# Performance work log

Measured on AMD Instinct MI355X. Metric: run time of the kernel, lower is better.

## Reference

```python
import jax, jax.numpy as jnp
import numpy as np

DIM = 2048
HEADS = 16
DIM_HEAD = 128
FF_MULT = 4
ATTN_INNER = HEADS * DIM_HEAD            # 2048
FF_INNER = DIM * FF_MULT                 # 8192
FUSED = ATTN_INNER + DIM_HEAD + DIM_HEAD + 2 * FF_INNER  # 18688
B, N = 2, 2048


def setup_inputs() -> dict:
    key = jax.random.key(0)
    k0, k1, k2, k3 = jax.random.split(key, 4)
    s = lambda fan_in: 1.0 / np.sqrt(fan_in)
    return {
        "x": jax.random.normal(k0, (B, N, DIM), jnp.float32),
        "gamma": jnp.ones((DIM,), jnp.float32),
        "beta": jnp.zeros((DIM,), jnp.float32),
        "w_fused": jax.random.normal(k1, (DIM, FUSED), jnp.float32) * s(DIM),
        "w_attn_out": jax.random.normal(k2, (ATTN_INNER, DIM), jnp.float32) * s(ATTN_INNER),
        "w_ff_out": jax.random.normal(k3, (FF_INNER, DIM), jnp.float32) * s(FF_INNER),
    }


def _rotate_half(t):
    t1, t2 = jnp.split(t, 2, axis=-1)
    return jnp.concatenate([-t2, t1], axis=-1)


def _rope(pos, t):
    # pos: [n, d] broadcast over leading dims of t (..., n, d)
    return t * jnp.cos(pos) + _rotate_half(t) * jnp.sin(pos)


def reference(x, gamma, beta, w_fused, w_attn_out, w_ff_out):
    b, n, d = x.shape
    # LayerNorm (eps = 1e-5, matching F.layer_norm default)
    mu = jnp.mean(x, axis=-1, keepdims=True)
    var = jnp.var(x, axis=-1, keepdims=True)
    h = (x - mu) * jax.lax.rsqrt(var + 1e-5) * gamma + beta

    # Fused projection feeding attention (multi-query) and parallel SwiGLU FF
    proj = h @ w_fused  # [b, n, FUSED]
    i0 = ATTN_INNER
    i1 = i0 + DIM_HEAD
    i2 = i1 + DIM_HEAD
    q, k, v, ff = jnp.split(proj, [i0, i1, i2], axis=-1)
    q = q.reshape(b, n, HEADS, DIM_HEAD).transpose(0, 2, 1, 3)  # [b, h, n, dh]

    # Rotary embedding: freqs duplicated, rotate-half application
    inv_freq = 1.0 / (10000.0 ** (jnp.arange(0, DIM_HEAD, 2, dtype=jnp.float32) / DIM_HEAD))
    freqs = jnp.arange(n, dtype=jnp.float32)[:, None] * inv_freq[None, :]
    pos = jnp.concatenate([freqs, freqs], axis=-1)  # [n, dh]
    q = _rope(pos, q)          # [b, h, n, dh]
    k = _rope(pos, k)          # [b, n, dh] (single KV head)

    # Multi-query causal attention
    scale = 1.0 / jnp.sqrt(jnp.asarray(DIM_HEAD, q.dtype))
    sim = jnp.einsum('bhid,bjd->bhij', q, k) * scale  # [b, h, n, n]
    causal = jnp.triu(jnp.ones((n, n), dtype=bool), 1)
    sim = jnp.where(causal, jnp.finfo(sim.dtype).min, sim)
    attn = jax.nn.softmax(sim, axis=-1)
    out = jnp.einsum('bhij,bjd->bhid', attn, v)       # [b, h, n, dh]
    out = out.transpose(0, 2, 1, 3).reshape(b, n, ATTN_INNER)

    # Parallel SwiGLU FF: chunk -> silu(gate) * x
    x_ff, gate = jnp.split(ff, 2, axis=-1)  # each [b, n, FF_INNER]
    ff_o = (jax.nn.silu(gate) * x_ff) @ w_ff_out

    return out @ w_attn_out + ff_o
```

## Files before the change

### kernel.cpp

```cpp
#include <hip/hip_runtime.h>
#include <hip/hip_bf16.h>
#include <math.h>

#define DIM 2048
#define HEADS 16
#define DH 128
#define ATTN_INNER 2048
#define FF_INNER 8192
#define FUSED_N 18688
#define QKV_N 2304
#define BATCH 2
#define SEQ 2048
#define ROWS (BATCH*SEQ)

typedef __attribute__((ext_vector_type(8))) __bf16 bf16x8;
typedef __attribute__((ext_vector_type(4))) float f32x4;

typedef __attribute__((address_space(1))) void* as1_void;
typedef __attribute__((address_space(3))) void* as3_void;

__device__ __forceinline__ void async16(const void* g, void* l) {
  __builtin_amdgcn_global_load_lds((as1_void)const_cast<void*>(g), (as3_void)l, 16, 0, 0);
}

__global__ __launch_bounds__(256) void ln_kernel(const float* __restrict__ x,
                                                 const float* __restrict__ gamma,
                                                 const float* __restrict__ beta,
                                                 __hip_bfloat16* __restrict__ hb) {
  const int row = blockIdx.x;
  const int t = threadIdx.x;
  const float4* x4 = (const float4*)(x + (size_t)row * DIM);
  float4 a = x4[t];
  float4 c = x4[t + 256];
  float s  = a.x + a.y + a.z + a.w + c.x + c.y + c.z + c.w;
  float ss = a.x*a.x + a.y*a.y + a.z*a.z + a.w*a.w +
             c.x*c.x + c.y*c.y + c.z*c.z + c.w*c.w;
  for (int off = 32; off > 0; off >>= 1) {
    s  += __shfl_down(s, off);
    ss += __shfl_down(ss, off);
  }
  __shared__ float red[8];
  int wv = t >> 6, lane = t & 63;
  if (lane == 0) { red[wv] = s; red[wv + 4] = ss; }
  __syncthreads();
  s  = red[0] + red[1] + red[2] + red[3];
  ss = red[4] + red[5] + red[6] + red[7];
  float mu  = s * (1.0f / DIM);
  float var = ss * (1.0f / DIM) - mu * mu;
  float rs  = rsqrtf(var + 1e-5f);
  __hip_bfloat16* o = hb + (size_t)row * DIM;
  float v0[4] = {a.x, a.y, a.z, a.w};
  float v1[4] = {c.x, c.y, c.z, c.w};
#pragma unroll
  for (int i = 0; i < 4; i++) {
    int c0 = t * 4 + i;
    int c1 = 1024 + t * 4 + i;
    o[c0] = __float2bfloat16((v0[i] - mu) * rs * gamma[c0] + beta[c0]);
    o[c1] = __float2bfloat16((v1[i] - mu) * rs * gamma[c1] + beta[c1]);
  }
}

__global__ __launch_bounds__(256) void tcvt_kernel(const float* __restrict__ src,
                                                   __hip_bfloat16* __restrict__ dst,
                                                   int R, int C) {
  __shared__ float tile[64][65];
  const int cb = blockIdx.x * 64, rb = blockIdx.y * 64;
  const int t = threadIdx.x;
  const int tc = t & 63, tr = t >> 6;
#pragma unroll
  for (int i = 0; i < 16; i++) {
    int r = tr + i * 4;
    tile[r][tc] = src[(size_t)(rb + r) * C + cb + tc];
  }
  __syncthreads();
#pragma unroll
  for (int i = 0; i < 16; i++) {
    int c = tr + i * 4;
    dst[(size_t)(cb + c) * R + rb + tc] = __float2bfloat16(tile[tc][c]);
  }
}

__global__ __launch_bounds__(256) void tbf16_kernel(const __hip_bfloat16* __restrict__ src, int lds_,
                                                    __hip_bfloat16* __restrict__ dst, int ldd,
                                                    int R, int C) {
  __shared__ __hip_bfloat16 tile[64][65];
  const int cb = blockIdx.x * 64, rb = blockIdx.y * 64;
  const int t = threadIdx.x;
  const int tc = t & 63, tr = t >> 6;
#pragma unroll
  for (int i = 0; i < 16; i++) {
    int r = tr + i * 4;
    tile[r][tc] = src[(size_t)(rb + r) * lds_ + cb + tc];
  }
  __syncthreads();
#pragma unroll
  for (int i = 0; i < 16; i++) {
    int c = tr + i * 4;
    dst[(size_t)(cb + c) * ldd + rb + tc] = tile[tc][c];
  }
}

__global__ __launch_bounds__(256) void rope_kernel(__hip_bfloat16* __restrict__ qkv) {
  const size_t tid = (size_t)blockIdx.x * 256 + threadIdx.x;
  const int d = tid & 63;
  const int u = (tid >> 6) % 17;
  const int row = tid / (17 * 64);
  const int n = row & (SEQ - 1);
  size_t base = (size_t)row * QKV_N + (u < 16 ? u * DH : ATTN_INNER);
  float inv = powf(10000.0f, -(float)d * (1.0f / 64.0f));
  float th = (float)n * inv;
  float cs = cosf(th), sn = sinf(th);
  float a = __bfloat162float(qkv[base + d]);
  float b = __bfloat162float(qkv[base + d + 64]);
  qkv[base + d]      = __float2bfloat16(a * cs - b * sn);
  qkv[base + d + 64] = __float2bfloat16(b * cs + a * sn);
}

template<int EPI>
__global__ __launch_bounds__(256) void gemm_bt(const __hip_bfloat16* __restrict__ A, int lda,
                                               const __hip_bfloat16* __restrict__ Bt, int ldb,
                                               void* __restrict__ Cptr, int ldc, int K) {
  __shared__ __hip_bfloat16 As[128 * 32];
  __shared__ __hip_bfloat16 Bs[128 * 32];
  const int tid = threadIdx.x;
  const int wv = tid >> 6, lane = tid & 63;
  const int quad = lane >> 4, l15 = lane & 15;
  const int m0 = blockIdx.y * 128, n0 = blockIdx.x * 128;
  const int wm = (wv >> 1) * 64, wn = (wv & 1) * 64;

  f32x4 acc[4][4];
#pragma unroll
  for (int i = 0; i < 4; i++)
#pragma unroll
    for (int j = 0; j < 4; j++) acc[i][j] = (f32x4){0.f, 0.f, 0.f, 0.f};

  for (int k0 = 0; k0 < K; k0 += 32) {
#pragma unroll
    for (int j = 0; j < 2; j++) {
      int q = wv * 2 + j;
      int e = q * 512 + lane * 8;
      int row = e >> 5, col = e & 31;
      async16(A  + (size_t)(m0 + row) * lda + k0 + col, As + q * 512);
      async16(Bt + (size_t)(n0 + row) * ldb + k0 + col, Bs + q * 512);
    }
    __syncthreads();
    bf16x8 af[4], bfr[4];
#pragma unroll
    for (int i = 0; i < 4; i++)
      af[i] = *(const bf16x8*)(As + (wm + i * 16 + l15) * 32 + quad * 8);
#pragma unroll
    for (int j = 0; j < 4; j++)
      bfr[j] = *(const bf16x8*)(Bs + (wn + j * 16 + l15) * 32 + quad * 8);
#pragma unroll
    for (int i = 0; i < 4; i++)
#pragma unroll
      for (int j = 0; j < 4; j++)
        acc[i][j] = __builtin_amdgcn_mfma_f32_16x16x32_bf16(af[i], bfr[j], acc[i][j], 0, 0, 0);
    __syncthreads();
  }

  if constexpr (EPI == 0 || EPI == 1) {
    __hip_bfloat16* C = (__hip_bfloat16*)Cptr;
#pragma unroll
    for (int i = 0; i < 4; i++) {
      int rowb = m0 + wm + i * 16 + quad * 4;
#pragma unroll
      for (int j = 0; j < 4; j++) {
        int col = n0 + wn + j * 16 + l15;
#pragma unroll
        for (int r = 0; r < 4; r++) {
          float v = acc[i][j][r];
          size_t idx = (size_t)(rowb + r) * ldc + col;
          if constexpr (EPI == 1) {
            float xf = __bfloat162float(C[idx]);
            v = v / (1.0f + expf(-v)) * xf;
          }
          C[idx] = __float2bfloat16(v);
        }
      }
    }
  } else {
    float* C = (float*)Cptr;
#pragma unroll
    for (int i = 0; i < 4; i++) {
      int rowb = m0 + wm + i * 16 + quad * 4;
#pragma unroll
      for (int j = 0; j < 4; j++) {
        int col = n0 + wn + j * 16 + l15;
#pragma unroll
        for (int r = 0; r < 4; r++) {
          size_t idx = (size_t)(rowb + r) * ldc + col;
          if constexpr (EPI == 3) C[idx] += acc[i][j][r];
          else                    C[idx]  = acc[i][j][r];
        }
      }
    }
  }
}

__global__ __launch_bounds__(256) void flash_kernel(const __hip_bfloat16* __restrict__ qkv,
                                                    const __hip_bfloat16* __restrict__ vt,
                                                    __hip_bfloat16* __restrict__ aob) {
  __shared__ __hip_bfloat16 Qs[128 * 128];
  __shared__ __hip_bfloat16 Ks[64 * 128];
  __shared__ __hip_bfloat16 Vts[128 * 64];
  __shared__ __hip_bfloat16 Ps[128 * 64];

  const int blk = blockIdx.x;
  const int bh = blk & 31;
  const int qi = blk >> 5;
  const int qt = (qi & 1) ? (qi >> 1) : (15 - (qi >> 1));
  const int bat = bh >> 4, h = bh & 15;

  const int tid = threadIdx.x;
  const int wv = tid >> 6, lane = tid & 63;
  const int quad = lane >> 4, l15 = lane & 15;
  const float scale = 0.08838834764831845f;

#pragma unroll
  for (int j = 0; j < 8; j++) {
    int is = wv * 8 + j;
    int e = is * 512 + lane * 8;
    int r = e >> 7, c = e & 127;
    async16(qkv + (size_t)(bat * SEQ + qt * 128 + r) * QKV_N + h * DH + c, Qs + is * 512);
  }

  f32x4 oacc[2][8];
#pragma unroll
  for (int i = 0; i < 2; i++)
#pragma unroll
    for (int j = 0; j < 8; j++) oacc[i][j] = (f32x4){0.f, 0.f, 0.f, 0.f};
  float mrow[2][4], lrow[2][4];
#pragma unroll
  for (int i = 0; i < 2; i++)
#pragma unroll
    for (int r = 0; r < 4; r++) { mrow[i][r] = -INFINITY; lrow[i][r] = 0.f; }

  const int jt_max = 2 * qt + 1;
  for (int jt = 0; jt <= jt_max; jt++) {
    __syncthreads();
#pragma unroll
    for (int j = 0; j < 4; j++) {
      int is = wv * 4 + j;
      int e = is * 512 + lane * 8;
      { int r = e >> 7, c = e & 127;
        async16(qkv + (size_t)(bat * SEQ + jt * 64 + r) * QKV_N + ATTN_INNER + c, Ks + is * 512); }
      { int d = e >> 6, jc = e & 63;
        async16(vt + (size_t)d * ROWS + bat * SEQ + jt * 64 + jc, Vts + is * 512); }
    }
    __syncthreads();

    f32x4 sacc[2][4];
#pragma unroll
    for (int i = 0; i < 2; i++)
#pragma unroll
      for (int j = 0; j < 4; j++) sacc[i][j] = (f32x4){0.f, 0.f, 0.f, 0.f};
#pragma unroll
    for (int kq = 0; kq < 4; kq++) {
      bf16x8 qa[2], kb[4];
#pragma unroll
      for (int i = 0; i < 2; i++)
        qa[i] = *(const bf16x8*)(Qs + (wv * 32 + i * 16 + l15) * 128 + kq * 32 + quad * 8);
#pragma unroll
      for (int j = 0; j < 4; j++)
        kb[j] = *(const bf16x8*)(Ks + (j * 16 + l15) * 128 + kq * 32 + quad * 8);
#pragma unroll
      for (int i = 0; i < 2; i++)
#pragma unroll
        for (int j = 0; j < 4; j++)
          sacc[i][j] = __builtin_amdgcn_mfma_f32_16x16x32_bf16(qa[i], kb[j], sacc[i][j], 0, 0, 0);
    }

#pragma unroll
    for (int i = 0; i < 2; i++) {
#pragma unroll
      for (int r = 0; r < 4; r++) {
        int row_g = qt * 128 + wv * 32 + i * 16 + quad * 4 + r;
        float mt = -INFINITY;
#pragma unroll
        for (int j = 0; j < 4; j++) {
          int col_g = jt * 64 + j * 16 + l15;
          float sv = sacc[i][j][r] * scale;
          if (col_g > row_g) sv = -INFINITY;
          sacc[i][j][r] = sv;
          mt = fmaxf(mt, sv);
        }
#pragma unroll
        for (int off = 1; off < 16; off <<= 1) mt = fmaxf(mt, __shfl_xor(mt, off));
        float mn = fmaxf(mrow[i][r], mt);
        float al = expf(mrow[i][r] - mn);
        float rs = 0.f;
#pragma unroll
        for (int j = 0; j < 4; j++) {
          float p = expf(sacc[i][j][r] - mn);
          sacc[i][j][r] = p;
          rs += p;
        }
#pragma unroll
        for (int off = 1; off < 16; off <<= 1) rs += __shfl_xor(rs, off);
        lrow[i][r] = lrow[i][r] * al + rs;
        mrow[i][r] = mn;
#pragma unroll
        for (int i2 = 0; i2 < 8; i2++) oacc[i][i2][r] *= al;
      }
    }

#pragma unroll
    for (int i = 0; i < 2; i++)
#pragma unroll
      for (int j = 0; j < 4; j++)
#pragma unroll
        for (int r = 0; r < 4; r++)
          Ps[(wv * 32 + i * 16 + quad * 4 + r) * 64 + j * 16 + l15] =
              __float2bfloat16(sacc[i][j][r]);
    __syncthreads();

#pragma unroll
    for (int kp = 0; kp < 2; kp++) {
      bf16x8 pa[2], vb[8];
#pragma unroll
      for (int i = 0; i < 2; i++)
        pa[i] = *(const bf16x8*)(Ps + (wv * 32 + i * 16 + l15) * 64 + kp * 32 + quad * 8);
#pragma unroll
      for (int i2 = 0; i2 < 8; i2++)
        vb[i2] = *(const bf16x8*)(Vts + (i2 * 16 + l15) * 64 + kp * 32 + quad * 8);
#pragma unroll
      for (int i = 0; i < 2; i++)
#pragma unroll
        for (int i2 = 0; i2 < 8; i2++)
          oacc[i][i2] = __builtin_amdgcn_mfma_f32_16x16x32_bf16(pa[i], vb[i2], oacc[i][i2], 0, 0, 0);
    }
  }

#pragma unroll
  for (int i = 0; i < 2; i++)
#pragma unroll
    for (int r = 0; r < 4; r++) {
      float inv = 1.0f / lrow[i][r];
      int row_g = bat * SEQ + qt * 128 + wv * 32 + i * 16 + quad * 4 + r;
#pragma unroll
      for (int i2 = 0; i2 < 8; i2++)
        aob[(size_t)row_g * ATTN_INNER + h * DH + i2 * 16 + l15] =
            __float2bfloat16(oacc[i][i2][r] * inv);
    }
}

extern "C" void kernel_launch(void* const* d_in, const int* in_sizes, int n_in,
                              void* d_out, int out_size, void* d_ws, size_t ws_size,
                              hipStream_t stream) {
  const float* x       = (const float*)d_in[0];
  const float* gamma   = (const float*)d_in[1];
  const float* beta    = (const float*)d_in[2];
  const float* w_fused = (const float*)d_in[3];
  const float* w_attn  = (const float*)d_in[4];
  const float* w_ff    = (const float*)d_in[5];
  float* out = (float*)d_out;
  char* ws = (char*)d_ws;

  size_t off = 0;
  auto alloc = [&](size_t bytes) {
    size_t o = off;
    off += (bytes + 255) & ~(size_t)255;
    return o;
  };
  __hip_bfloat16* hb   = (__hip_bfloat16*)(ws + alloc((size_t)ROWS * DIM * 2));
  __hip_bfloat16* wfbt = (__hip_bfloat16*)(ws + alloc((size_t)FUSED_N * DIM * 2));
  __hip_bfloat16* qkvb = (__hip_bfloat16*)(ws + alloc((size_t)ROWS * QKV_N * 2));
  __hip_bfloat16* gb   = (__hip_bfloat16*)(ws + alloc((size_t)ROWS * FF_INNER * 2));
  __hip_bfloat16* wat  = (__hip_bfloat16*)(ws + alloc((size_t)DIM * ATTN_INNER * 2));
  __hip_bfloat16* wfot = (__hip_bfloat16*)(ws + alloc((size_t)DIM * FF_INNER * 2));
  __hip_bfloat16* vt   = (__hip_bfloat16*)(ws + alloc((size_t)DH * ROWS * 2));
  __hip_bfloat16* aob  = (__hip_bfloat16*)(ws + alloc((size_t)ROWS * ATTN_INNER * 2));

  ln_kernel<<<ROWS, 256, 0, stream>>>(x, gamma, beta, hb);

  tcvt_kernel<<<dim3(FUSED_N / 64, DIM / 64), 256, 0, stream>>>(w_fused, wfbt, DIM, FUSED_N);
  tcvt_kernel<<<dim3(DIM / 64, ATTN_INNER / 64), 256, 0, stream>>>(w_attn, wat, ATTN_INNER, DIM);
  tcvt_kernel<<<dim3(DIM / 64, FF_INNER / 64), 256, 0, stream>>>(w_ff, wfot, FF_INNER, DIM);

  gemm_bt<0><<<dim3(QKV_N / 128, ROWS / 128), 256, 0, stream>>>(hb, DIM, wfbt, DIM, qkvb, QKV_N, DIM);

  rope_kernel<<<(ROWS * 17 * 64) / 256, 256, 0, stream>>>(qkvb);

  tbf16_kernel<<<dim3(DH / 64, ROWS / 64), 256, 0, stream>>>(qkvb + ATTN_INNER + DH, QKV_N, vt, ROWS, ROWS, DH);

  flash_kernel<<<512, 256, 0, stream>>>(qkvb, vt, aob);

  gemm_bt<0><<<dim3(FF_INNER / 128, ROWS / 128), 256, 0, stream>>>(
      hb, DIM, wfbt + (size_t)QKV_N * DIM, DIM, gb, FF_INNER, DIM);
  gemm_bt<1><<<dim3(FF_INNER / 128, ROWS / 128), 256, 0, stream>>>(
      hb, DIM, wfbt + (size_t)(QKV_N + FF_INNER) * DIM, DIM, gb, FF_INNER, DIM);

  gemm_bt<2><<<dim3(DIM / 128, ROWS / 128), 256, 0, stream>>>(aob, ATTN_INNER, wat, ATTN_INNER, out, DIM, ATTN_INNER);
  gemm_bt<3><<<dim3(DIM / 128, ROWS / 128), 256, 0, stream>>>(gb, FF_INNER, wfot, FF_INNER, out, DIM, FF_INNER);

  (void)in_sizes; (void)n_in; (void)out_size; (void)ws_size;
}
```

Baseline: 1.324 ms.

## Fuse SwiGLU GEMMs and output GEMMs, add tile swizzle and wider K steps

Replaces the generic templated GEMM with three specialised kernels. The FF value and gate projections are computed in one kernel, which keeps both accumulators and applies SiLU-gating in registers, so the intermediate x_ff is never written to or read back from memory. The attention-out and FF-out projections are accumulated in one kernel, removing the fp32 output read-modify-write. It also adds grouped tile swizzling for L2 reuse, a 64-wide K step per barrier, an occupancy hint, and vectorised weight-transpose loads and stores. Together these raise register pressure, and the fused output GEMM has fewer, longer-running blocks.

```diff
diff --git a/kernel.cpp b/kernel.cpp
--- a/kernel.cpp
+++ b/kernel.cpp
@@ -21,6 +21,16 @@
 
 __device__ __forceinline__ void async16(const void* g, void* l) {
   __builtin_amdgcn_global_load_lds((as1_void)const_cast<void*>(g), (as3_void)l, 16, 0, 0);
+}
+
+__device__ __forceinline__ void swizzle_tile(int& tm, int& tn) {
+  const int num_n = gridDim.x;
+  const int pid = blockIdx.y * num_n + blockIdx.x;
+  const int group = 8 * num_n;
+  const int gid = pid / group;
+  const int rem = pid % group;
+  tm = gid * 8 + (rem % 8);
+  tn = rem / 8;
 }
 
 __global__ __launch_bounds__(256) void ln_kernel(const float* __restrict__ x,
@@ -66,17 +76,24 @@
   __shared__ float tile[64][65];
   const int cb = blockIdx.x * 64, rb = blockIdx.y * 64;
   const int t = threadIdx.x;
-  const int tc = t & 63, tr = t >> 6;
-#pragma unroll
-  for (int i = 0; i < 16; i++) {
-    int r = tr + i * 4;
-    tile[r][tc] = src[(size_t)(rb + r) * C + cb + tc];
+  const int lr = t >> 4, lc4 = (t & 15) * 4;
+#pragma unroll
+  for (int i = 0; i < 4; i++) {
+    float4 v = *(const float4*)&src[(size_t)(rb + lr + i * 16) * C + cb + lc4];
+    tile[lr + i * 16][lc4 + 0] = v.x;
+    tile[lr + i * 16][lc4 + 1] = v.y;
+    tile[lr + i * 16][lc4 + 2] = v.z;
+    tile[lr + i * 16][lc4 + 3] = v.w;
   }
   __syncthreads();
-#pragma unroll
-  for (int i = 0; i < 16; i++) {
-    int c = tr + i * 4;
-    dst[(size_t)(cb + c) * R + rb + tc] = __float2bfloat16(tile[tc][c]);
+  const int tcc = t & 31, trc = t >> 5;
+#pragma unroll
+  for (int i = 0; i < 8; i++) {
+    int c = trc + i * 8;
+    __hip_bfloat162 pk;
+    pk.x = __float2bfloat16(tile[2 * tcc][c]);
+    pk.y = __float2bfloat16(tile[2 * tcc + 1][c]);
+    *(__hip_bfloat162*)&dst[(size_t)(cb + c) * R + rb + 2 * tcc] = pk;
   }
 }
 
@@ -116,84 +133,185 @@
   qkv[base + d + 64] = __float2bfloat16(b * cs + a * sn);
 }
 
-template<int EPI>
-__global__ __launch_bounds__(256) void gemm_bt(const __hip_bfloat16* __restrict__ A, int lda,
-                                               const __hip_bfloat16* __restrict__ Bt, int ldb,
-                                               void* __restrict__ Cptr, int ldc, int K) {
-  __shared__ __hip_bfloat16 As[128 * 32];
-  __shared__ __hip_bfloat16 Bs[128 * 32];
+__global__ __launch_bounds__(256, 3) void gemm_qkv(const __hip_bfloat16* __restrict__ A,
+                                                   const __hip_bfloat16* __restrict__ Bt,
+                                                   __hip_bfloat16* __restrict__ C) {
+  __shared__ __hip_bfloat16 As[2][128 * 32];
+  __shared__ __hip_bfloat16 Bs[2][128 * 32];
   const int tid = threadIdx.x;
   const int wv = tid >> 6, lane = tid & 63;
   const int quad = lane >> 4, l15 = lane & 15;
-  const int m0 = blockIdx.y * 128, n0 = blockIdx.x * 128;
+  int tm, tn; swizzle_tile(tm, tn);
+  const int m0 = tm * 128, n0 = tn * 128;
   const int wm = (wv >> 1) * 64, wn = (wv & 1) * 64;
-
-  f32x4 acc[4][4];
-#pragma unroll
-  for (int i = 0; i < 4; i++)
-#pragma unroll
-    for (int j = 0; j < 4; j++) acc[i][j] = (f32x4){0.f, 0.f, 0.f, 0.f};
-
-  for (int k0 = 0; k0 < K; k0 += 32) {
+  const int srow = lane >> 2, scol = (lane & 3) * 8;
+
+  f32x4 acc[4][4] = {};
+  for (int k0 = 0; k0 < DIM; k0 += 64) {
+#pragma unroll
+    for (int h = 0; h < 2; h++)
+#pragma unroll
+      for (int j = 0; j < 2; j++) {
+        int q = wv * 2 + j;
+        int row = q * 16 + srow;
+        async16(A  + (size_t)(m0 + row) * DIM + k0 + h * 32 + scol, &As[h][q * 512]);
+        async16(Bt + (size_t)(n0 + row) * DIM + k0 + h * 32 + scol, &Bs[h][q * 512]);
+      }
+    __syncthreads();
+#pragma unroll
+    for (int h = 0; h < 2; h++) {
+      bf16x8 af[4], bfr[4];
+#pragma unroll
+      for (int i = 0; i < 4; i++)
+        af[i] = *(const bf16x8*)(&As[h][(wm + i * 16 + l15) * 32 + quad * 8]);
+#pragma unroll
+      for (int j = 0; j < 4; j++)
+        bfr[j] = *(const bf16x8*)(&Bs[h][(wn + j * 16 + l15) * 32 + quad * 8]);
+#pragma unroll
+      for (int i = 0; i < 4; i++)
+#pragma unroll
+        for (int j = 0; j < 4; j++)
+          acc[i][j] = __builtin_amdgcn_mfma_f32_16x16x32_bf16(af[i], bfr[j], acc[i][j], 0, 0, 0);
+    }
+    __syncthreads();
+  }
+#pragma unroll
+  for (int i = 0; i < 4; i++) {
+    int rowb = m0 + wm + i * 16 + quad * 4;
+#pragma unroll
+    for (int j = 0; j < 4; j++) {
+      int col = n0 + wn + j * 16 + l15;
+#pragma unroll
+      for (int r = 0; r < 4; r++)
+        C[(size_t)(rowb + r) * QKV_N + col] = __float2bfloat16(acc[i][j][r]);
+    }
+  }
+}
+
+__global__ __launch_bounds__(256, 3) void gemm_ff(const __hip_bfloat16* __restrict__ A,
+                                                  const __hip_bfloat16* __restrict__ W,
+                                                  __hip_bfloat16* __restrict__ G) {
+  __shared__ __hip_bfloat16 As[2][128 * 32];
+  __shared__ __hip_bfloat16 Bs[2][128 * 32];
+  const int tid = threadIdx.x;
+  const int wv = tid >> 6, lane = tid & 63;
+  const int quad = lane >> 4, l15 = lane & 15;
+  int tm, tn; swizzle_tile(tm, tn);
+  const int m0 = tm * 128, n0 = tn * 64;
+  const int wm = (wv >> 1) * 64, wn2 = (wv & 1) * 32;
+  const int srow = lane >> 2, scol = (lane & 3) * 8;
+
+  f32x4 ax[4][2] = {};
+  f32x4 ag[4][2] = {};
+  for (int k0 = 0; k0 < DIM; k0 += 64) {
+#pragma unroll
+    for (int h = 0; h < 2; h++)
+#pragma unroll
+      for (int j = 0; j < 2; j++) {
+        int q = wv * 2 + j;
+        int row = q * 16 + srow;
+        async16(A + (size_t)(m0 + row) * DIM + k0 + h * 32 + scol, &As[h][q * 512]);
+        int wr = (row < 64) ? (QKV_N + n0 + row)
+                            : (QKV_N + FF_INNER + n0 + row - 64);
+        async16(W + (size_t)wr * DIM + k0 + h * 32 + scol, &Bs[h][q * 512]);
+      }
+    __syncthreads();
+#pragma unroll
+    for (int h = 0; h < 2; h++) {
+      bf16x8 af[4], bx[2], bg[2];
+#pragma unroll
+      for (int i = 0; i < 4; i++)
+        af[i] = *(const bf16x8*)(&As[h][(wm + i * 16 + l15) * 32 + quad * 8]);
+#pragma unroll
+      for (int j = 0; j < 2; j++) {
+        bx[j] = *(const bf16x8*)(&Bs[h][(wn2 + j * 16 + l15) * 32 + quad * 8]);
+        bg[j] = *(const bf16x8*)(&Bs[h][(64 + wn2 + j * 16 + l15) * 32 + quad * 8]);
+      }
+#pragma unroll
+      for (int i = 0; i < 4; i++)
+#pragma unroll
+        for (int j = 0; j < 2; j++) {
+          ax[i][j] = __builtin_amdgcn_mfma_f32_16x16x32_bf16(af[i], bx[j], ax[i][j], 0, 0, 0);
+          ag[i][j] = __builtin_amdgcn_mfma_f32_16x16x32_bf16(af[i], bg[j], ag[i][j], 0, 0, 0);
+        }
+    }
+    __syncthreads();
+  }
+#pragma unroll
+  for (int i = 0; i < 4; i++) {
+    int rowb = m0 + wm + i * 16 + quad * 4;
 #pragma unroll
     for (int j = 0; j < 2; j++) {
-      int q = wv * 2 + j;
-      int e = q * 512 + lane * 8;
-      int row = e >> 5, col = e & 31;
-      async16(A  + (size_t)(m0 + row) * lda + k0 + col, As + q * 512);
-      async16(Bt + (size_t)(n0 + row) * ldb + k0 + col, Bs + q * 512);
-    }
-    __syncthreads();
-    bf16x8 af[4], bfr[4];
-#pragma unroll
-    for (int i = 0; i < 4; i++)
-      af[i] = *(const bf16x8*)(As + (wm + i * 16 + l15) * 32 + quad * 8);
-#pragma unroll
-    for (int j = 0; j < 4; j++)
-      bfr[j] = *(const bf16x8*)(Bs + (wn + j * 16 + l15) * 32 + quad * 8);
-#pragma unroll
-    for (int i = 0; i < 4; i++)
-#pragma unroll
-      for (int j = 0; j < 4; j++)
-        acc[i][j] = __builtin_amdgcn_mfma_f32_16x16x32_bf16(af[i], bfr[j], acc[i][j], 0, 0, 0);
-    __syncthreads();
-  }
-
-  if constexpr (EPI == 0 || EPI == 1) {
-    __hip_bfloat16* C = (__hip_bfloat16*)Cptr;
-#pragma unroll
-    for (int i = 0; i < 4; i++) {
-      int rowb = m0 + wm + i * 16 + quad * 4;
-#pragma unroll
-      for (int j = 0; j < 4; j++) {
-        int col = n0 + wn + j * 16 + l15;
-#pragma unroll
-        for (int r = 0; r < 4; r++) {
-          float v = acc[i][j][r];
-          size_t idx = (size_t)(rowb + r) * ldc + col;
-          if constexpr (EPI == 1) {
-            float xf = __bfloat162float(C[idx]);
-            v = v / (1.0f + expf(-v)) * xf;
-          }
-          C[idx] = __float2bfloat16(v);
+      int col = n0 + wn2 + j * 16 + l15;
+#pragma unroll
+      for (int r = 0; r < 4; r++) {
+        float xv = ax[i][j][r];
+        float gv = ag[i][j][r];
+        float o = gv / (1.0f + expf(-gv)) * xv;
+        G[(size_t)(rowb + r) * FF_INNER + col] = __float2bfloat16(o);
+      }
+    }
+  }
+}
+
+__global__ __launch_bounds__(256, 3) void gemm_out(const __hip_bfloat16* __restrict__ A0,
+                                                   const __hip_bfloat16* __restrict__ B0,
+                                                   const __hip_bfloat16* __restrict__ A1,
+                                                   const __hip_bfloat16* __restrict__ B1,
+                                                   float* __restrict__ C) {
+  __shared__ __hip_bfloat16 As[2][128 * 32];
+  __shared__ __hip_bfloat16 Bs[2][128 * 32];
+  const int tid = threadIdx.x;
+  const int wv = tid >> 6, lane = tid & 63;
+  const int quad = lane >> 4, l15 = lane & 15;
+  int tm, tn; swizzle_tile(tm, tn);
+  const int m0 = tm * 128, n0 = tn * 128;
+  const int wm = (wv >> 1) * 64, wn = (wv & 1) * 64;
+  const int srow = lane >> 2, scol = (lane & 3) * 8;
+
+  f32x4 acc[4][4] = {};
+  for (int p = 0; p < 2; p++) {
+    const __hip_bfloat16* A = p ? A1 : A0;
+    const __hip_bfloat16* B = p ? B1 : B0;
+    const int K = p ? FF_INNER : ATTN_INNER;
+    for (int k0 = 0; k0 < K; k0 += 64) {
+#pragma unroll
+      for (int h = 0; h < 2; h++)
+#pragma unroll
+        for (int j = 0; j < 2; j++) {
+          int q = wv * 2 + j;
+          int row = q * 16 + srow;
+          async16(A + (size_t)(m0 + row) * K + k0 + h * 32 + scol, &As[h][q * 512]);
+          async16(B + (size_t)(n0 + row) * K + k0 + h * 32 + scol, &Bs[h][q * 512]);
         }
+      __syncthreads();
+#pragma unroll
+      for (int h = 0; h < 2; h++) {
+        bf16x8 af[4], bfr[4];
+#pragma unroll
+        for (int i = 0; i < 4; i++)
+          af[i] = *(const bf16x8*)(&As[h][(wm + i * 16 + l15) * 32 + quad * 8]);
+#pragma unroll
+        for (int j = 0; j < 4; j++)
+          bfr[j] = *(const bf16x8*)(&Bs[h][(wn + j * 16 + l15) * 32 + quad * 8]);
+#pragma unroll
+        for (int i = 0; i < 4; i++)
+#pragma unroll
+          for (int j = 0; j < 4; j++)
+            acc[i][j] = __builtin_amdgcn_mfma_f32_16x16x32_bf16(af[i], bfr[j], acc[i][j], 0, 0, 0);
       }
-    }
-  } else {
-    float* C = (float*)Cptr;
-#pragma unroll
-    for (int i = 0; i < 4; i++) {
-      int rowb = m0 + wm + i * 16 + quad * 4;
-#pragma unroll
-      for (int j = 0; j < 4; j++) {
-        int col = n0 + wn + j * 16 + l15;
-#pragma unroll
-        for (int r = 0; r < 4; r++) {
-          size_t idx = (size_t)(rowb + r) * ldc + col;
-          if constexpr (EPI == 3) C[idx] += acc[i][j][r];
-          else                    C[idx]  = acc[i][j][r];
-        }
-      }
+      __syncthreads();
+    }
+  }
+#pragma unroll
+  for (int i = 0; i < 4; i++) {
+    int rowb = m0 + wm + i * 16 + quad * 4;
+#pragma unroll
+    for (int j = 0; j < 4; j++) {
+      int col = n0 + wn + j * 16 + l15;
+#pragma unroll
+      for (int r = 0; r < 4; r++)
+        C[(size_t)(rowb + r) * DIM + col] = acc[i][j][r];
     }
   }
 }
@@ -378,7 +496,7 @@
   tcvt_kernel<<<dim3(DIM / 64, ATTN_INNER / 64), 256, 0, stream>>>(w_attn, wat, ATTN_INNER, DIM);
   tcvt_kernel<<<dim3(DIM / 64, FF_INNER / 64), 256, 0, stream>>>(w_ff, wfot, FF_INNER, DIM);
 
-  gemm_bt<0><<<dim3(QKV_N / 128, ROWS / 128), 256, 0, stream>>>(hb, DIM, wfbt, DIM, qkvb, QKV_N, DIM);
+  gemm_qkv<<<dim3(QKV_N / 128, ROWS / 128), 256, 0, stream>>>(hb, wfbt, qkvb);
 
   rope_kernel<<<(ROWS * 17 * 64) / 256, 256, 0, stream>>>(qkvb);
 
@@ -386,13 +504,9 @@
 
   flash_kernel<<<512, 256, 0, stream>>>(qkvb, vt, aob);
 
-  gemm_bt<0><<<dim3(FF_INNER / 128, ROWS / 128), 256, 0, stream>>>(
-      hb, DIM, wfbt + (size_t)QKV_N * DIM, DIM, gb, FF_INNER, DIM);
-  gemm_bt<1><<<dim3(FF_INNER / 128, ROWS / 128), 256, 0, stream>>>(
-      hb, DIM, wfbt + (size_t)(QKV_N + FF_INNER) * DIM, DIM, gb, FF_INNER, DIM);
-
-  gemm_bt<2><<<dim3(DIM / 128, ROWS / 128), 256, 0, stream>>>(aob, ATTN_INNER, wat, ATTN_INNER, out, DIM, ATTN_INNER);
-  gemm_bt<3><<<dim3(DIM / 128, ROWS / 128), 256, 0, stream>>>(gb, FF_INNER, wfot, FF_INNER, out, DIM, FF_INNER);
+  gemm_ff<<<dim3(FF_INNER / 64, ROWS / 128), 256, 0, stream>>>(hb, wfbt, gb);
+
+  gemm_out<<<dim3(DIM / 128, ROWS / 128), 256, 0, stream>>>(aob, wat, gb, wfot, out);
 
   (void)in_sizes; (void)n_in; (void)out_size; (void)ws_size;
 }
```

Result: faster. 1.150 ms (-13.1%).
